# Performance work log

Hardware: AMD Instinct MI355X
Metric: run time of the kernel (lower is better)

The kernel has to match this reference:

```python
import jax, jax.numpy as jnp
import numpy as np

N_ENTITY, N_REL, DIM, H = 500000, 32, 64, 2
N_ITEM, N_MEM, BATCH, HIST = 10000, 32, 4096, 50


def setup_inputs() -> dict:
    key = jax.random.key(0)
    ks = jax.random.split(key, 10)
    return {
        "entity_emb": jax.random.normal(ks[0], (N_ENTITY, DIM), jnp.float32) * 0.05,
        "relation_emb": jax.random.normal(ks[1], (N_REL, DIM), jnp.float32) * 0.05,
        "W_w": jax.random.normal(ks[2], (1, 3 * DIM), jnp.float32) * 0.05,
        "W_b": jnp.zeros((1,), jnp.float32),
        "item_ids": jax.random.randint(ks[3], (N_ITEM,), 0, N_ENTITY, jnp.int32),
        "heads": jax.random.randint(ks[4], (H, N_ITEM, N_MEM), 0, N_ENTITY, jnp.int32),
        "relations": jax.random.randint(ks[5], (H, N_ITEM, N_MEM), 0, N_REL, jnp.int32),
        "tails": jax.random.randint(ks[6], (H, N_ITEM, N_MEM), 0, N_ENTITY, jnp.int32),
        "records_idx": jax.random.randint(ks[7], (BATCH, HIST), 0, N_ITEM, jnp.int32),
        "items": jax.random.randint(ks[8], (BATCH,), 0, N_ENTITY, jnp.int32),
    }


def reference(entity_emb, relation_emb, W_w, W_b, item_ids, heads, relations, tails, records_idx, items):
    d = entity_emb.shape[1]
    # Split the Linear(3d->1) weight so we never materialize the [n_item,m,3d] concat.
    w_h, w_r, w_t = W_w[0, :d], W_w[0, d:2 * d], W_w[0, 2 * d:]
    # Hop-0 item embedding (base entity embedding of each candidate item).
    acc = entity_emb[item_ids]  # [n_item, d]
    for h in range(heads.shape[0]):
        te = entity_emb[tails[h]]  # [n_item, m, d]
        logits = (entity_emb[heads[h]] @ w_h
                  + relation_emb[relations[h]] @ w_r
                  + te @ w_t + W_b[0])  # [n_item, m]
        # Original: sigmoid then softmax over the memory axis.
        pi = jax.nn.softmax(jax.nn.sigmoid(logits), axis=1)[..., None]
        acc = acc + (pi * te).sum(axis=1)
    # User embedding = sum of (hop-enhanced) item embeddings over history records.
    user_emb = acc[records_idx].sum(axis=1)  # [B, d]
    pair_item = entity_emb[items]            # [B, d] (raw entity embedding)
    return jax.nn.sigmoid(jnp.sum(user_emb * pair_item, axis=-1))
```

## Files before the change

### kernel.cpp

```cpp
#include <hip/hip_runtime.h>
#include <math.h>

#define DIM    64
#define N_MEM  32
#define N_ITEM 10000
#define HOPS   2
#define BATCH  4096
#define HIST   50

typedef float4 f4;


__global__ __launch_bounds__(256) void ripple_stage1(
    const float* __restrict__ entity_emb,
    const float* __restrict__ relation_emb,
    const float* __restrict__ W_w,
    const float* __restrict__ W_b,
    const int*   __restrict__ heads,
    const int*   __restrict__ relations,
    const int*   __restrict__ tails,
    float*       __restrict__ accp)
{
    const int wave = (blockIdx.x * blockDim.x + threadIdx.x) >> 6;
    const int lane = threadIdx.x & 63;
    if (wave >= HOPS * N_ITEM) return;
    const int h = wave < N_ITEM ? 0 : 1;
    const int i = wave - h * N_ITEM;
    const int g = lane >> 4;
    const int p = lane & 15;

    const f4* __restrict__ E4 = (const f4*)entity_emb;
    const f4* __restrict__ R4 = (const f4*)relation_emb;
    const f4* __restrict__ W4 = (const f4*)W_w;

    const f4 wh = W4[p];
    const f4 wr = W4[16 + p];
    const f4 wt = W4[32 + p];
    const float bias = W_b[0];

    const int base = wave * N_MEM + g;

    int hi[8], ri[8], ti[8];
#pragma unroll
    for (int k = 0; k < 8; ++k) {
        hi[k] = heads[base + 4 * k];
        ri[k] = relations[base + 4 * k];
        ti[k] = tails[base + 4 * k];
    }

    f4 he[8], re[8], te[8];
#pragma unroll
    for (int k = 0; k < 8; ++k) he[k] = E4[(size_t)hi[k] * 16 + p];
#pragma unroll
    for (int k = 0; k < 8; ++k) re[k] = R4[(size_t)ri[k] * 16 + p];
#pragma unroll
    for (int k = 0; k < 8; ++k) te[k] = E4[(size_t)ti[k] * 16 + p];

    float part[8];
#pragma unroll
    for (int k = 0; k < 8; ++k) {
        part[k] = he[k].x * wh.x + he[k].y * wh.y + he[k].z * wh.z + he[k].w * wh.w
                + re[k].x * wr.x + re[k].y * wr.y + re[k].z * wr.z + re[k].w * wr.w
                + te[k].x * wt.x + te[k].y * wt.y + te[k].z * wt.z + te[k].w * wt.w;
    }

    float e[8];
    float se = 0.f;
#pragma unroll
    for (int k = 0; k < 8; ++k) {
        float v = part[k];
        v += __shfl_xor(v, 1, 64);
        v += __shfl_xor(v, 2, 64);
        v += __shfl_xor(v, 4, 64);
        v += __shfl_xor(v, 8, 64);
        const float logit = v + bias;
        const float sig   = 1.f / (1.f + __expf(-logit));
        const float ex    = __expf(sig);
        e[k] = ex;
        se += ex;
    }
    se += __shfl_xor(se, 16, 64);
    se += __shfl_xor(se, 32, 64);
    const float inv = 1.f / se;

    f4 acc = {0.f, 0.f, 0.f, 0.f};
#pragma unroll
    for (int k = 0; k < 8; ++k) {
        const float w = e[k] * inv;
        acc.x += w * te[k].x;
        acc.y += w * te[k].y;
        acc.z += w * te[k].z;
        acc.w += w * te[k].w;
    }

    acc.x += __shfl_xor(acc.x, 16, 64);
    acc.x += __shfl_xor(acc.x, 32, 64);
    acc.y += __shfl_xor(acc.y, 16, 64);
    acc.y += __shfl_xor(acc.y, 32, 64);
    acc.z += __shfl_xor(acc.z, 16, 64);
    acc.z += __shfl_xor(acc.z, 32, 64);
    acc.w += __shfl_xor(acc.w, 16, 64);
    acc.w += __shfl_xor(acc.w, 32, 64);
    if (g == 0) ((f4*)accp)[((size_t)i * 2 + h) * 16 + p] = acc;
}

__global__ __launch_bounds__(256) void ripple_fold(
    const float* __restrict__ entity_emb,
    const int*   __restrict__ item_ids,
    const float* __restrict__ accp,
    float*       __restrict__ folded)
{
    const int t = blockIdx.x * blockDim.x + threadIdx.x;
    if (t >= N_ITEM * 16) return;
    const int i = t >> 4;
    const int p = t & 15;
    const f4* __restrict__ E4 = (const f4*)entity_emb;
    const f4* __restrict__ A4 = (const f4*)accp;
    const f4 a  = A4[(size_t)i * 32 + p];
    const f4 b  = A4[(size_t)i * 32 + 16 + p];
    const f4 it = E4[(size_t)item_ids[i] * 16 + p];
    f4 r;
    r.x = it.x + a.x + b.x;
    r.y = it.y + a.y + b.y;
    r.z = it.z + a.z + b.z;
    r.w = it.w + a.w + b.w;
    ((f4*)folded)[(size_t)i * 16 + p] = r;
}

__global__ __launch_bounds__(256) void ripple_stage2(
    const float* __restrict__ entity_emb,
    const int*   __restrict__ records_idx,
    const int*   __restrict__ items,
    const float* __restrict__ folded,
    float*       __restrict__ out)
{
    const int wave = (blockIdx.x * blockDim.x + threadIdx.x) >> 6;
    const int lane = threadIdx.x & 63;
    if (wave >= BATCH) return;
    const int b = wave;
    const int g = lane >> 4;
    const int p = lane & 15;

    const f4* __restrict__ A4 = (const f4*)folded;
    const f4* __restrict__ E4 = (const f4*)entity_emb;

    const int rb = b * HIST;
    int idx[13];
    float wgt[13];
#pragma unroll
    for (int k = 0; k < 13; ++k) {
        const int j  = 4 * k + g;
        const int jc = j < HIST ? j : (HIST - 1);
        wgt[k] = j < HIST ? 1.f : 0.f;
        idx[k] = records_idx[rb + jc];
    }

    f4 user = {0.f, 0.f, 0.f, 0.f};
#pragma unroll
    for (int k = 0; k < 13; ++k) {
        const f4 r = A4[(size_t)idx[k] * 16 + p];
        user.x += wgt[k] * r.x;
        user.y += wgt[k] * r.y;
        user.z += wgt[k] * r.z;
        user.w += wgt[k] * r.w;
    }
    user.x += __shfl_xor(user.x, 16, 64);
    user.x += __shfl_xor(user.x, 32, 64);
    user.y += __shfl_xor(user.y, 16, 64);
    user.y += __shfl_xor(user.y, 32, 64);
    user.z += __shfl_xor(user.z, 16, 64);
    user.z += __shfl_xor(user.z, 32, 64);
    user.w += __shfl_xor(user.w, 16, 64);
    user.w += __shfl_xor(user.w, 32, 64);

    const f4 pair = E4[(size_t)items[b] * 16 + p];
    float dot = user.x * pair.x + user.y * pair.y + user.z * pair.z + user.w * pair.w;
    dot += __shfl_xor(dot, 1, 64);
    dot += __shfl_xor(dot, 2, 64);
    dot += __shfl_xor(dot, 4, 64);
    dot += __shfl_xor(dot, 8, 64);
    if (lane == 0) out[b] = 1.f / (1.f + __expf(-dot));
}

extern "C" void kernel_launch(void* const* d_in, const int* in_sizes, int n_in,
                              void* d_out, int out_size, void* d_ws, size_t ws_size,
                              hipStream_t stream) {
    const float* entity_emb   = (const float*)d_in[0];
    const float* relation_emb = (const float*)d_in[1];
    const float* W_w          = (const float*)d_in[2];
    const float* W_b          = (const float*)d_in[3];
    const int*   item_ids     = (const int*)d_in[4];
    const int*   heads        = (const int*)d_in[5];
    const int*   relations    = (const int*)d_in[6];
    const int*   tails        = (const int*)d_in[7];
    const int*   records_idx  = (const int*)d_in[8];
    const int*   items        = (const int*)d_in[9];
    float* out = (float*)d_out;

    float* accp   = (float*)d_ws;
    float* folded = accp + (size_t)N_ITEM * HOPS * DIM;

    const int waves1  = HOPS * N_ITEM;
    const int blocks1 = (waves1 + 3) / 4;
    ripple_stage1<<<blocks1, 256, 0, stream>>>(entity_emb, relation_emb, W_w, W_b,
                                               heads, relations, tails, accp);

    const int blocksF = (N_ITEM * 16 + 255) / 256;
    ripple_fold<<<blocksF, 256, 0, stream>>>(entity_emb, item_ids, accp, folded);

    const int blocks2 = (BATCH + 3) / 4;
    ripple_stage2<<<blocks2, 256, 0, stream>>>(entity_emb, records_idx, items,
                                               folded, out);
}
```

Before: 228.3 us.

## Precompute per-entity attention dot products to avoid gathering head embeddings

A new kernel projects every entity row onto the head and tail weight slices, and every relation row onto the relation slice, and stores these scalars. The memory kernel then gathers only three scalars per memory slot to form the logits, so it no longer fetches full head and relation embedding rows. Each wave now gathers the tail rows once, using shuffled indices and softmax weights. The trade is a full sequential pass over the 500k-entity table, plus an extra launch and workspace, in exchange for roughly halving the random row gathers.

```diff
diff --git a/kernel.cpp b/kernel.cpp
--- a/kernel.cpp
+++ b/kernel.cpp
@@ -1,24 +1,71 @@
 #include <hip/hip_runtime.h>
 #include <math.h>
 
-#define DIM    64
-#define N_MEM  32
-#define N_ITEM 10000
-#define HOPS   2
-#define BATCH  4096
-#define HIST   50
+#define DIM      64
+#define N_MEM    32
+#define N_ENTITY 500000
+#define N_REL    32
+#define N_ITEM   10000
+#define HOPS     2
+#define BATCH    4096
+#define HIST     50
 
 typedef float4 f4;
 
-
-__global__ __launch_bounds__(256) void ripple_stage1(
+__global__ __launch_bounds__(256) void ripple_dots(
     const float* __restrict__ entity_emb,
     const float* __restrict__ relation_emb,
     const float* __restrict__ W_w,
+    float* __restrict__ hdot,
+    float* __restrict__ tdot,
+    float* __restrict__ rdot)
+{
+    const int wave = (blockIdx.x * blockDim.x + threadIdx.x) >> 6;
+    const int lane = threadIdx.x & 63;
+    const int g = lane >> 4;
+    const int p = lane & 15;
+    const int row = wave * 4 + g;
+    if (row >= N_ENTITY + N_REL) return;
+
+    const f4* __restrict__ W4 = (const f4*)W_w;
+
+    if (row < N_ENTITY) {
+        const f4 wh = W4[p];
+        const f4 wt = W4[32 + p];
+        const f4 e4 = ((const f4*)entity_emb)[(size_t)row * 16 + p];
+        float vh = e4.x * wh.x + e4.y * wh.y + e4.z * wh.z + e4.w * wh.w;
+        float vt = e4.x * wt.x + e4.y * wt.y + e4.z * wt.z + e4.w * wt.w;
+        vh += __shfl_xor(vh, 1, 64);
+        vh += __shfl_xor(vh, 2, 64);
+        vh += __shfl_xor(vh, 4, 64);
+        vh += __shfl_xor(vh, 8, 64);
+        vt += __shfl_xor(vt, 1, 64);
+        vt += __shfl_xor(vt, 2, 64);
+        vt += __shfl_xor(vt, 4, 64);
+        vt += __shfl_xor(vt, 8, 64);
+        if (p == 0) { hdot[row] = vh; tdot[row] = vt; }
+    } else {
+        const int r = row - N_ENTITY;
+        const f4 wr = W4[16 + p];
+        const f4 r4 = ((const f4*)relation_emb)[(size_t)r * 16 + p];
+        float vr = r4.x * wr.x + r4.y * wr.y + r4.z * wr.z + r4.w * wr.w;
+        vr += __shfl_xor(vr, 1, 64);
+        vr += __shfl_xor(vr, 2, 64);
+        vr += __shfl_xor(vr, 4, 64);
+        vr += __shfl_xor(vr, 8, 64);
+        if (p == 0) rdot[r] = vr;
+    }
+}
+
+__global__ __launch_bounds__(256) void ripple_stage1(
     const float* __restrict__ W_b,
     const int*   __restrict__ heads,
     const int*   __restrict__ relations,
     const int*   __restrict__ tails,
+    const float* __restrict__ entity_emb,
+    const float* __restrict__ hdot,
+    const float* __restrict__ tdot,
+    const float* __restrict__ rdot,
     float*       __restrict__ accp)
 {
     const int wave = (blockIdx.x * blockDim.x + threadIdx.x) >> 6;
@@ -28,69 +75,51 @@
     const int i = wave - h * N_ITEM;
     const int g = lane >> 4;
     const int p = lane & 15;
-
-    const f4* __restrict__ E4 = (const f4*)entity_emb;
-    const f4* __restrict__ R4 = (const f4*)relation_emb;
-    const f4* __restrict__ W4 = (const f4*)W_w;
-
-    const f4 wh = W4[p];
-    const f4 wr = W4[16 + p];
-    const f4 wt = W4[32 + p];
+    const int m = lane & 31;
+
+    const int base = wave * N_MEM;
     const float bias = W_b[0];
 
-    const int base = wave * N_MEM + g;
-
-    int hi[8], ri[8], ti[8];
-#pragma unroll
-    for (int k = 0; k < 8; ++k) {
-        hi[k] = heads[base + 4 * k];
-        ri[k] = relations[base + 4 * k];
-        ti[k] = tails[base + 4 * k];
-    }
-
-    f4 he[8], re[8], te[8];
-#pragma unroll
-    for (int k = 0; k < 8; ++k) he[k] = E4[(size_t)hi[k] * 16 + p];
-#pragma unroll
-    for (int k = 0; k < 8; ++k) re[k] = R4[(size_t)ri[k] * 16 + p];
-#pragma unroll
-    for (int k = 0; k < 8; ++k) te[k] = E4[(size_t)ti[k] * 16 + p];
-
-    float part[8];
-#pragma unroll
-    for (int k = 0; k < 8; ++k) {
-        part[k] = he[k].x * wh.x + he[k].y * wh.y + he[k].z * wh.z + he[k].w * wh.w
-                + re[k].x * wr.x + re[k].y * wr.y + re[k].z * wr.z + re[k].w * wr.w
-                + te[k].x * wt.x + te[k].y * wt.y + te[k].z * wt.z + te[k].w * wt.w;
-    }
-
-    float e[8];
-    float se = 0.f;
-#pragma unroll
-    for (int k = 0; k < 8; ++k) {
-        float v = part[k];
-        v += __shfl_xor(v, 1, 64);
-        v += __shfl_xor(v, 2, 64);
-        v += __shfl_xor(v, 4, 64);
-        v += __shfl_xor(v, 8, 64);
-        const float logit = v + bias;
-        const float sig   = 1.f / (1.f + __expf(-logit));
-        const float ex    = __expf(sig);
-        e[k] = ex;
-        se += ex;
-    }
+    const int hidx = heads[base + m];
+    const int ridx = relations[base + m];
+    const int tidx = tails[base + m];
+    const float lh = hdot[hidx];
+    const float lr = rdot[ridx];
+    const float lt = tdot[tidx];
+
+    const float logit = lh + lr + lt + bias;
+    const float sig   = 1.f / (1.f + __expf(-logit));
+    float e = (lane < 32) ? __expf(sig) : 0.f;
+
+    float se = e;
+    se += __shfl_xor(se, 1, 64);
+    se += __shfl_xor(se, 2, 64);
+    se += __shfl_xor(se, 4, 64);
+    se += __shfl_xor(se, 8, 64);
     se += __shfl_xor(se, 16, 64);
     se += __shfl_xor(se, 32, 64);
-    const float inv = 1.f / se;
+    const float pi = e / se;
+
+    int   tk[8];
+    float pk[8];
+#pragma unroll
+    for (int k = 0; k < 8; ++k) {
+        tk[k] = __shfl(tidx, 4 * k + g, 64);
+        pk[k] = __shfl(pi,   4 * k + g, 64);
+    }
+
+    const f4* __restrict__ E4 = (const f4*)entity_emb;
+    f4 te[8];
+#pragma unroll
+    for (int k = 0; k < 8; ++k) te[k] = E4[(size_t)tk[k] * 16 + p];
 
     f4 acc = {0.f, 0.f, 0.f, 0.f};
 #pragma unroll
     for (int k = 0; k < 8; ++k) {
-        const float w = e[k] * inv;
-        acc.x += w * te[k].x;
-        acc.y += w * te[k].y;
-        acc.z += w * te[k].z;
-        acc.w += w * te[k].w;
+        acc.x += pk[k] * te[k].x;
+        acc.y += pk[k] * te[k].y;
+        acc.z += pk[k] * te[k].z;
+        acc.w += pk[k] * te[k].w;
     }
 
     acc.x += __shfl_xor(acc.x, 16, 64);
@@ -197,13 +226,21 @@
     const int*   items        = (const int*)d_in[9];
     float* out = (float*)d_out;
 
-    float* accp   = (float*)d_ws;
+    float* hdot   = (float*)d_ws;
+    float* tdot   = hdot + N_ENTITY;
+    float* rdot   = tdot + N_ENTITY;
+    float* accp   = rdot + N_REL;
     float* folded = accp + (size_t)N_ITEM * HOPS * DIM;
+
+    const int wavesD  = (N_ENTITY + N_REL + 3) / 4;
+    const int blocksD = (wavesD + 3) / 4;
+    ripple_dots<<<blocksD, 256, 0, stream>>>(entity_emb, relation_emb, W_w,
+                                             hdot, tdot, rdot);
 
     const int waves1  = HOPS * N_ITEM;
     const int blocks1 = (waves1 + 3) / 4;
-    ripple_stage1<<<blocks1, 256, 0, stream>>>(entity_emb, relation_emb, W_w, W_b,
-                                               heads, relations, tails, accp);
+    ripple_stage1<<<blocks1, 256, 0, stream>>>(W_b, heads, relations, tails,
+                                               entity_emb, hdot, tdot, rdot, accp);
 
     const int blocksF = (N_ITEM * 16 + 255) / 256;
     ripple_fold<<<blocksF, 256, 0, stream>>>(entity_emb, item_ids, accp, folded);
```

Measured after the change: 241.0 us. +5.6%, slower.

## Gather fp16 copy of entity table and precompute relation logit terms

Applied to the files above, without the earlier changes.

Adds a pre-pass that converts the whole entity embedding table to half precision and precomputes each relation's dot product with its weight slice. Stage1 then gathers 128-byte fp16 rows for heads and tails, with 8 lanes per memory slot instead of 16, and looks up one scalar per relation instead of gathering relation rows. The aim is to halve the bytes moved by the random gathers. In exchange, every call now streams the full 500k-row fp32 table once and writes a half-size copy, and fp16 rounding adds numerical error.

```diff
diff --git a/kernel.cpp b/kernel.cpp
--- a/kernel.cpp
+++ b/kernel.cpp
@@ -1,107 +1,146 @@
 #include <hip/hip_runtime.h>
+#include <hip/hip_fp16.h>
 #include <math.h>
 
-#define DIM    64
-#define N_MEM  32
-#define N_ITEM 10000
-#define HOPS   2
-#define BATCH  4096
-#define HIST   50
+#define DIM      64
+#define N_MEM    32
+#define N_ENTITY 500000
+#define N_REL    32
+#define N_ITEM   10000
+#define HOPS     2
+#define BATCH    4096
+#define HIST     50
 
 typedef float4 f4;
 
-
-__global__ __launch_bounds__(256) void ripple_stage1(
+__device__ __forceinline__ void unpack8(const uint4& r, float f[8]) {
+    union { unsigned int u; __half2 h; } c;
+    c.u = r.x; f[0] = __low2float(c.h); f[1] = __high2float(c.h);
+    c.u = r.y; f[2] = __low2float(c.h); f[3] = __high2float(c.h);
+    c.u = r.z; f[4] = __low2float(c.h); f[5] = __high2float(c.h);
+    c.u = r.w; f[6] = __low2float(c.h); f[7] = __high2float(c.h);
+}
+
+__global__ __launch_bounds__(256) void ripple_convert(
     const float* __restrict__ entity_emb,
     const float* __restrict__ relation_emb,
+    const float* __restrict__ W_w,
+    unsigned int* __restrict__ eh,
+    float* __restrict__ rdot)
+{
+    const int wave = (blockIdx.x * blockDim.x + threadIdx.x) >> 6;
+    const int lane = threadIdx.x & 63;
+    const int g = lane >> 4;
+    const int p = lane & 15;
+    const int row = wave * 4 + g;
+    if (row < N_ENTITY) {
+        const f4 e4 = ((const f4*)entity_emb)[(size_t)row * 16 + p];
+        const __half2 lo = __floats2half2_rn(e4.x, e4.y);
+        const __half2 hi = __floats2half2_rn(e4.z, e4.w);
+        uint2 pk;
+        pk.x = *(const unsigned int*)&lo;
+        pk.y = *(const unsigned int*)&hi;
+        ((uint2*)eh)[(size_t)row * 16 + p] = pk;
+    } else if (row < N_ENTITY + N_REL) {
+        const int r = row - N_ENTITY;
+        const f4 wr = ((const f4*)W_w)[16 + p];
+        const f4 r4 = ((const f4*)relation_emb)[(size_t)r * 16 + p];
+        float vr = r4.x * wr.x + r4.y * wr.y + r4.z * wr.z + r4.w * wr.w;
+        vr += __shfl_xor(vr, 1, 64);
+        vr += __shfl_xor(vr, 2, 64);
+        vr += __shfl_xor(vr, 4, 64);
+        vr += __shfl_xor(vr, 8, 64);
+        if (p == 0) rdot[r] = vr;
+    }
+}
+
+__global__ __launch_bounds__(256) void ripple_stage1(
     const float* __restrict__ W_w,
     const float* __restrict__ W_b,
     const int*   __restrict__ heads,
     const int*   __restrict__ relations,
     const int*   __restrict__ tails,
+    const unsigned int* __restrict__ eh,
+    const float* __restrict__ rdot,
     float*       __restrict__ accp)
 {
     const int wave = (blockIdx.x * blockDim.x + threadIdx.x) >> 6;
     const int lane = threadIdx.x & 63;
     if (wave >= HOPS * N_ITEM) return;
-    const int h = wave < N_ITEM ? 0 : 1;
-    const int i = wave - h * N_ITEM;
-    const int g = lane >> 4;
-    const int p = lane & 15;
-
-    const f4* __restrict__ E4 = (const f4*)entity_emb;
-    const f4* __restrict__ R4 = (const f4*)relation_emb;
+    const int h  = wave < N_ITEM ? 0 : 1;
+    const int i  = wave - h * N_ITEM;
+    const int g8 = lane >> 3;
+    const int p8 = lane & 7;
+
+    const int base = wave * N_MEM;
+
+    int hk[4], tk[4], rk[4];
+#pragma unroll
+    for (int k = 0; k < 4; ++k) {
+        hk[k] = heads[base + 8 * k + g8];
+        tk[k] = tails[base + 8 * k + g8];
+        rk[k] = relations[base + 8 * k + g8];
+    }
+
+    const uint4* __restrict__ E = (const uint4*)eh;
+    uint4 hraw[4], traw[4];
+#pragma unroll
+    for (int k = 0; k < 4; ++k) hraw[k] = E[(size_t)hk[k] * 8 + p8];
+#pragma unroll
+    for (int k = 0; k < 4; ++k) traw[k] = E[(size_t)tk[k] * 8 + p8];
+
     const f4* __restrict__ W4 = (const f4*)W_w;
-
-    const f4 wh = W4[p];
-    const f4 wr = W4[16 + p];
-    const f4 wt = W4[32 + p];
+    const f4 wh0 = W4[p8 * 2],      wh1 = W4[p8 * 2 + 1];
+    const f4 wt0 = W4[32 + p8 * 2], wt1 = W4[32 + p8 * 2 + 1];
     const float bias = W_b[0];
-
-    const int base = wave * N_MEM + g;
-
-    int hi[8], ri[8], ti[8];
-#pragma unroll
-    for (int k = 0; k < 8; ++k) {
-        hi[k] = heads[base + 4 * k];
-        ri[k] = relations[base + 4 * k];
-        ti[k] = tails[base + 4 * k];
-    }
-
-    f4 he[8], re[8], te[8];
-#pragma unroll
-    for (int k = 0; k < 8; ++k) he[k] = E4[(size_t)hi[k] * 16 + p];
-#pragma unroll
-    for (int k = 0; k < 8; ++k) re[k] = R4[(size_t)ri[k] * 16 + p];
-#pragma unroll
-    for (int k = 0; k < 8; ++k) te[k] = E4[(size_t)ti[k] * 16 + p];
-
-    float part[8];
-#pragma unroll
-    for (int k = 0; k < 8; ++k) {
-        part[k] = he[k].x * wh.x + he[k].y * wh.y + he[k].z * wh.z + he[k].w * wh.w
-                + re[k].x * wr.x + re[k].y * wr.y + re[k].z * wr.z + re[k].w * wr.w
-                + te[k].x * wt.x + te[k].y * wt.y + te[k].z * wt.z + te[k].w * wt.w;
-    }
-
-    float e[8];
+    float lr[4];
+#pragma unroll
+    for (int k = 0; k < 4; ++k) lr[k] = rdot[rk[k]];
+
+    float tef[4][8];
+    float e[4];
     float se = 0.f;
 #pragma unroll
-    for (int k = 0; k < 8; ++k) {
-        float v = part[k];
+    for (int k = 0; k < 4; ++k) {
+        float hf[8];
+        unpack8(hraw[k], hf);
+        unpack8(traw[k], tef[k]);
+        float v = hf[0] * wh0.x + hf[1] * wh0.y + hf[2] * wh0.z + hf[3] * wh0.w
+                + hf[4] * wh1.x + hf[5] * wh1.y + hf[6] * wh1.z + hf[7] * wh1.w
+                + tef[k][0] * wt0.x + tef[k][1] * wt0.y + tef[k][2] * wt0.z + tef[k][3] * wt0.w
+                + tef[k][4] * wt1.x + tef[k][5] * wt1.y + tef[k][6] * wt1.z + tef[k][7] * wt1.w;
         v += __shfl_xor(v, 1, 64);
         v += __shfl_xor(v, 2, 64);
         v += __shfl_xor(v, 4, 64);
-        v += __shfl_xor(v, 8, 64);
-        const float logit = v + bias;
+        const float logit = v + lr[k] + bias;
         const float sig   = 1.f / (1.f + __expf(-logit));
-        const float ex    = __expf(sig);
-        e[k] = ex;
-        se += ex;
-    }
+        e[k] = __expf(sig);
+        se += e[k];
+    }
+    se += __shfl_xor(se, 8, 64);
     se += __shfl_xor(se, 16, 64);
     se += __shfl_xor(se, 32, 64);
     const float inv = 1.f / se;
 
-    f4 acc = {0.f, 0.f, 0.f, 0.f};
-#pragma unroll
-    for (int k = 0; k < 8; ++k) {
+    float acc8[8] = {0.f, 0.f, 0.f, 0.f, 0.f, 0.f, 0.f, 0.f};
+#pragma unroll
+    for (int k = 0; k < 4; ++k) {
         const float w = e[k] * inv;
-        acc.x += w * te[k].x;
-        acc.y += w * te[k].y;
-        acc.z += w * te[k].z;
-        acc.w += w * te[k].w;
-    }
-
-    acc.x += __shfl_xor(acc.x, 16, 64);
-    acc.x += __shfl_xor(acc.x, 32, 64);
-    acc.y += __shfl_xor(acc.y, 16, 64);
-    acc.y += __shfl_xor(acc.y, 32, 64);
-    acc.z += __shfl_xor(acc.z, 16, 64);
-    acc.z += __shfl_xor(acc.z, 32, 64);
-    acc.w += __shfl_xor(acc.w, 16, 64);
-    acc.w += __shfl_xor(acc.w, 32, 64);
-    if (g == 0) ((f4*)accp)[((size_t)i * 2 + h) * 16 + p] = acc;
+#pragma unroll
+        for (int j = 0; j < 8; ++j) acc8[j] += w * tef[k][j];
+    }
+#pragma unroll
+    for (int j = 0; j < 8; ++j) {
+        acc8[j] += __shfl_xor(acc8[j], 8, 64);
+        acc8[j] += __shfl_xor(acc8[j], 16, 64);
+        acc8[j] += __shfl_xor(acc8[j], 32, 64);
+    }
+    if (g8 == 0) {
+        f4 s0 = {acc8[0], acc8[1], acc8[2], acc8[3]};
+        f4 s1 = {acc8[4], acc8[5], acc8[6], acc8[7]};
+        ((f4*)accp)[((size_t)i * 2 + h) * 16 + lane * 2]     = s0;
+        ((f4*)accp)[((size_t)i * 2 + h) * 16 + lane * 2 + 1] = s1;
+    }
 }
 
 __global__ __launch_bounds__(256) void ripple_fold(
@@ -197,13 +236,21 @@
     const int*   items        = (const int*)d_in[9];
     float* out = (float*)d_out;
 
-    float* accp   = (float*)d_ws;
-    float* folded = accp + (size_t)N_ITEM * HOPS * DIM;
+    unsigned int* eh   = (unsigned int*)d_ws;
+    float* rdot        = (float*)(eh + (size_t)N_ENTITY * 32);
+    float* accp        = rdot + N_REL;
+    float* folded      = accp + (size_t)N_ITEM * HOPS * DIM;
+
+    const int rowsC   = N_ENTITY + N_REL;
+    const int wavesC  = (rowsC + 3) / 4;
+    const int blocksC = (wavesC + 3) / 4;
+    ripple_convert<<<blocksC, 256, 0, stream>>>(entity_emb, relation_emb, W_w,
+                                                eh, rdot);
 
     const int waves1  = HOPS * N_ITEM;
     const int blocks1 = (waves1 + 3) / 4;
-    ripple_stage1<<<blocks1, 256, 0, stream>>>(entity_emb, relation_emb, W_w, W_b,
-                                               heads, relations, tails, accp);
+    ripple_stage1<<<blocks1, 256, 0, stream>>>(W_w, W_b, heads, relations, tails,
+                                               eh, rdot, accp);
 
     const int blocksF = (N_ITEM * 16 + 255) / 256;
     ripple_fold<<<blocksF, 256, 0, stream>>>(entity_emb, item_ids, accp, folded);
```

Measured after the change: 241.9 us. 5.9% more time.
